# Kernel tuning notes

Measured on AMD Instinct MI355X. Metric: run time of the kernel, lower is better.

Reference implementation:

```python
import jax, jax.numpy as jnp
import numpy as np

B, T, N, CD, D = 8, 16, 256, 1280, 1024   # batch, frames, feats/frame, condition_dim, dim
H, DH, DEPTH, Q = 16, 64, 6, 16           # heads, dim_head, depth, latents per frame
FF = 4 * D


def setup_inputs() -> dict:
    key = jax.random.key(0)
    ks = iter(jax.random.split(key, 40))
    w = lambda shp: jax.random.normal(next(ks), shp, jnp.float32) * 0.02
    return dict(
        x_f=jax.random.normal(next(ks), (B, T, N, CD), jnp.float32),
        goal_w1=w((CD, 2 * D)), goal_b1=jnp.zeros((2 * D,), jnp.float32),
        goal_w2=w((2 * D, D)), goal_b2=jnp.zeros((D,), jnp.float32),
        latents=jax.random.normal(next(ks), (T, Q, D), jnp.float32),
        time_pos_emb=jax.random.normal(next(ks), (T, 1, D), jnp.float32),
        ln_media_g=jnp.ones((DEPTH, D), jnp.float32), ln_media_b=jnp.zeros((DEPTH, D), jnp.float32),
        ln_lat_g=jnp.ones((DEPTH, D), jnp.float32), ln_lat_b=jnp.zeros((DEPTH, D), jnp.float32),
        wq=w((DEPTH, D, H * DH)), wk=w((DEPTH, D, H * DH)), wv=w((DEPTH, D, H * DH)),
        wo=w((DEPTH, H * DH, D)),
        ffn_ln_g=jnp.ones((DEPTH, D), jnp.float32), ffn_ln_b=jnp.zeros((DEPTH, D), jnp.float32),
        ffn_w1=w((DEPTH, D, FF)), ffn_b1=jnp.zeros((DEPTH, FF), jnp.float32),
        ffn_w2=w((DEPTH, FF, D)), ffn_b2=jnp.zeros((DEPTH, D), jnp.float32),
        final_g=jnp.ones((D,), jnp.float32), final_b=jnp.zeros((D,), jnp.float32),
    )


def layer_norm(x, g, b, eps=1e-5):
    m = jnp.mean(x, axis=-1, keepdims=True)
    v = jnp.mean(jnp.square(x - m), axis=-1, keepdims=True)
    return (x - m) * jax.lax.rsqrt(v + eps) * g + b


def reference(x_f, goal_w1, goal_b1, goal_w2, goal_b2, latents, time_pos_emb,
              ln_media_g, ln_media_b, ln_lat_g, ln_lat_b, wq, wk, wv, wo,
              ffn_ln_g, ffn_ln_b, ffn_w1, ffn_b1, ffn_w2, ffn_b2, final_g, final_b):
    scale = DH ** -0.5
    # goal embedding: Linear -> GELU(exact) -> Linear, then add time positional embedding
    h = jax.nn.gelu(x_f @ goal_w1 + goal_b1, approximate=False) @ goal_w2 + goal_b2  # (B,T,N,D)
    h = h + time_pos_emb[None]                                                       # (T,1,D) broadcast
    feats = h.reshape(B * T, N, D)
    x = jnp.broadcast_to(latents[None], (B, T, Q, D)).reshape(B * T, Q, D)
    for i in range(DEPTH):
        f = layer_norm(feats, ln_media_g[i], ln_media_b[i])
        lat = layer_norm(x, ln_lat_g[i], ln_lat_b[i])
        q = (lat @ wq[i]).reshape(B * T, Q, H, DH).transpose(0, 2, 1, 3) * scale  # bhqd
        kv = jnp.concatenate([f, lat], axis=1)                                    # (BT, N+Q, D)
        k = (kv @ wk[i]).reshape(B * T, N + Q, H, DH).transpose(0, 2, 1, 3)       # bhfd
        v = (kv @ wv[i]).reshape(B * T, N + Q, H, DH).transpose(0, 2, 1, 3)
        sim = jnp.einsum('bhqd,bhfd->bhqf', q, k)
        alphas = jax.nn.softmax(sim, axis=-1)  # matches amax-subtract + softmax
        o = jnp.einsum('bhqf,bhfd->bhqd', alphas, v)
        o = o.transpose(0, 2, 1, 3).reshape(B * T, Q, H * DH)
        x = x + o @ wo[i]
        y = layer_norm(x, ffn_ln_g[i], ffn_ln_b[i])
        x = x + jax.nn.gelu(y @ ffn_w1[i] + ffn_b1[i], approximate=False) @ ffn_w2[i] + ffn_b2[i]
    x = x.reshape(B, T * Q, D)
    return layer_norm(x, final_g, final_b)
```

## Files before the change

kernel.cpp:

```cpp
#include <hip/hip_runtime.h>
#include <math.h>

#define DEV __device__ __forceinline__

typedef __attribute__((ext_vector_type(8))) short short8;
typedef __attribute__((ext_vector_type(4))) short short4v;
typedef __attribute__((ext_vector_type(4))) float f32x4;
typedef __attribute__((ext_vector_type(8))) __bf16 bf16x8;

DEV float bf2f(unsigned short u) {
    union { unsigned int i; float f; } c; c.i = ((unsigned int)u) << 16; return c.f;
}
DEV unsigned short f2bf(float f) {
    union { float f; unsigned int i; } c; c.f = f;
    unsigned int u = c.i;
    u += 0x7fffu + ((u >> 16) & 1u);
    return (unsigned short)(u >> 16);
}
DEV float gelu_exact(float x) { return 0.5f * x * (1.0f + erff(x * 0.70710678118654752f)); }

DEV f32x4 MF(bf16x8 a, bf16x8 b, f32x4 c) {
    return __builtin_amdgcn_mfma_f32_16x16x32_bf16(a, b, c, 0, 0, 0);
}

#define GLL16(g, l)                                                                   \
    __builtin_amdgcn_global_load_lds(                                                \
        (const __attribute__((address_space(1))) unsigned int*)(g),                  \
        (__attribute__((address_space(3))) unsigned int*)(l), 16, 0, 0)

__global__ __launch_bounds__(256)
void transpose_w(const float* __restrict__ in, unsigned short* __restrict__ out,
                 const float* __restrict__ rowscale, float uscale,
                 int K, int N, size_t inStride, size_t outStride, int scaleStride)
{
    __shared__ float tile[64][65];
    in  += (size_t)blockIdx.z * inStride;
    out += (size_t)blockIdx.z * outStride;
    const int k0 = blockIdx.y * 64, n0 = blockIdx.x * 64;
    const int tid = threadIdx.x;
    const int c = tid & 63;
#pragma unroll
    for (int i = 0; i < 16; ++i) {
        int rr = (i << 2) + (tid >> 6);
        float v = in[(size_t)(k0 + rr) * N + n0 + c];
        if (rowscale) v *= rowscale[(size_t)blockIdx.z * scaleStride + k0 + rr];
        tile[rr][c] = v * uscale;
    }
    __syncthreads();
#pragma unroll
    for (int i = 0; i < 16; ++i) {
        int rr = (i << 2) + (tid >> 6);
        out[(size_t)(n0 + rr) * K + k0 + c] = f2bf(tile[c][rr]);
    }
}

__global__ __launch_bounds__(256)
void fold_bias(const float* __restrict__ wk, const float* __restrict__ wv,
               const float* __restrict__ bmed, float* __restrict__ biaskv)
{
    const int d = blockIdx.x >> 3;
    const int rem = blockIdx.x & 7;
    const int part = rem >> 2;
    const int chunk = rem & 3;
    const float* w = (part ? wv : wk) + (size_t)d * 1024 * 1024 + chunk * 256 + threadIdx.x;
    const float* b = bmed + d * 1024;
    float acc = 0.f;
    for (int r = 0; r < 1024; ++r) acc += b[r] * w[(size_t)r * 1024];
    biaskv[d * 2048 + part * 1024 + chunk * 256 + threadIdx.x] = acc;
}

__global__ __launch_bounds__(256)
void convert_bf16(const float* __restrict__ in, unsigned short* __restrict__ out, size_t n4)
{
    size_t i = (size_t)blockIdx.x * 256 + threadIdx.x;
    if (i >= n4) return;
    float4 v = ((const float4*)in)[i];
    ushort4 u;
    u.x = f2bf(v.x); u.y = f2bf(v.y); u.z = f2bf(v.z); u.w = f2bf(v.w);
    ((ushort4*)out)[i] = u;
}

__global__ __launch_bounds__(256)
void init_x(const float* __restrict__ lat, float* __restrict__ x)
{
    const int row = blockIdx.x;
    ((float4*)x)[(size_t)row * 256 + threadIdx.x] =
        ((const float4*)lat)[(size_t)(row & 255) * 256 + threadIdx.x];
}

template<bool AFFINE, bool OUTBF>
__global__ __launch_bounds__(256)
void ln_k(const float* __restrict__ in, const float* __restrict__ g,
          const float* __restrict__ b, void* __restrict__ out)
{
    const int row = blockIdx.x;
    const int tid = threadIdx.x;
    float4 v = ((const float4*)(in + (size_t)row * 1024))[tid];
    float s  = v.x + v.y + v.z + v.w;
    float ss = v.x * v.x + v.y * v.y + v.z * v.z + v.w * v.w;
#pragma unroll
    for (int o = 32; o > 0; o >>= 1) { s += __shfl_down(s, o); ss += __shfl_down(ss, o); }
    __shared__ float red[8];
    if ((tid & 63) == 0) { red[tid >> 6] = s; red[4 + (tid >> 6)] = ss; }
    __syncthreads();
    const float sum  = red[0] + red[1] + red[2] + red[3];
    const float ssum = red[4] + red[5] + red[6] + red[7];
    const float mean = sum * (1.0f / 1024.0f);
    const float var  = ssum * (1.0f / 1024.0f) - mean * mean;
    const float rs   = rsqrtf(var + 1e-5f);
    float o0 = (v.x - mean) * rs, o1 = (v.y - mean) * rs;
    float o2 = (v.z - mean) * rs, o3 = (v.w - mean) * rs;
    if (AFFINE) {
        float4 gv = ((const float4*)g)[tid];
        float4 bv = ((const float4*)b)[tid];
        o0 = o0 * gv.x + bv.x; o1 = o1 * gv.y + bv.y;
        o2 = o2 * gv.z + bv.z; o3 = o3 * gv.w + bv.w;
    }
    if (OUTBF) {
        ushort4 u; u.x = f2bf(o0); u.y = f2bf(o1); u.z = f2bf(o2); u.w = f2bf(o3);
        ((ushort4*)out)[(size_t)row * 256 + tid] = u;
    } else {
        float4 ov; ov.x = o0; ov.y = o1; ov.z = o2; ov.w = o3;
        ((float4*)out)[(size_t)row * 256 + tid] = ov;
    }
}

enum { E_BF16 = 0, E_BIAS_BF16, E_BIAS_GELU_BF16, E_BIAS_TPOS_F32, E_ADD_F32, E_BIAS_ADD_F32 };

template<int EPI>
__global__ __launch_bounds__(256, 2)
void gemm_bt(const unsigned short* __restrict__ A, const unsigned short* __restrict__ Bt,
             void* __restrict__ Out,
             const float* __restrict__ bias, const float* __restrict__ addsrc,
             const float* __restrict__ tpos,
             int M, int N, int K)
{
    __shared__ unsigned short lds[2 * 128 * 64];
    const int tid  = threadIdx.x;
    const int wave = tid >> 6, lane = tid & 63;
    const int nbx  = N >> 7;

    const int nwg = gridDim.x;
    int bid = blockIdx.x;
    int wg = ((nwg & 7) == 0) ? ((bid & 7) * (nwg >> 3) + (bid >> 3)) : bid;
    const int by = wg / nbx, bx = wg % nbx;

    const int swz = ((lane & 7) ^ (lane >> 3)) * 8;
    const unsigned short* gA = A  + (size_t)(by * 128 + (lane >> 3)) * K + swz;
    const unsigned short* gB = Bt + (size_t)(bx * 128 + (lane >> 3)) * K + swz;

    const int wr = wave >> 1, wc = wave & 1;
    f32x4 acc[4][4] = {};

    unsigned short* ldsA = lds;
    unsigned short* ldsB = lds + 128 * 64;

    const int off0 = (((lane >> 4)    ) ^ (lane & 7)) * 8;
    const int off1 = (((lane >> 4) | 4) ^ (lane & 7)) * 8;
    const unsigned short* la = ldsA + (wr * 64 + (lane & 15)) * 64;
    const unsigned short* lb = ldsB + (wc * 64 + (lane & 15)) * 64;

    for (int kt = 0; kt < K; kt += 64) {
#pragma unroll
        for (int j = 0; j < 4; ++j) {
            const int chunk = (j << 2) + wave;
            GLL16(gA + (size_t)chunk * 8 * K + kt, ldsA + chunk * 512);
            GLL16(gB + (size_t)chunk * 8 * K + kt, ldsB + chunk * 512);
        }
        __syncthreads();
#pragma unroll
        for (int kk = 0; kk < 2; ++kk) {
            const int offk = kk ? off1 : off0;
            bf16x8 a[4], b[4];
#pragma unroll
            for (int m = 0; m < 4; ++m) a[m] = *(const bf16x8*)(la + m * 1024 + offk);
#pragma unroll
            for (int n = 0; n < 4; ++n) b[n] = *(const bf16x8*)(lb + n * 1024 + offk);
#pragma unroll
            for (int m = 0; m < 4; ++m)
#pragma unroll
                for (int n = 0; n < 4; ++n)
                    acc[m][n] = MF(a[m], b[n], acc[m][n]);
        }
        __syncthreads();
    }

    const int r0 = by * 128 + wr * 64 + (lane >> 4) * 4;
    const int c0 = bx * 128 + wc * 64 + (lane & 15);
#pragma unroll
    for (int m = 0; m < 4; ++m) {
#pragma unroll
        for (int n = 0; n < 4; ++n) {
            const int c = c0 + n * 16;
#pragma unroll
            for (int j = 0; j < 4; ++j) {
                const int r = r0 + m * 16 + j;
                float v = acc[m][n][j];
                if (EPI == E_BIAS_BF16 || EPI == E_BIAS_GELU_BF16 ||
                    EPI == E_BIAS_TPOS_F32 || EPI == E_BIAS_ADD_F32)
                    v += bias[c];
                if (EPI == E_BIAS_GELU_BF16) v = gelu_exact(v);
                if (EPI == E_BIAS_TPOS_F32)  v += tpos[(((unsigned)r >> 8) & 15) * 1024 + c];
                if (EPI == E_ADD_F32 || EPI == E_BIAS_ADD_F32) v += addsrc[(size_t)r * N + c];
                if (EPI == E_BIAS_TPOS_F32 || EPI == E_ADD_F32 || EPI == E_BIAS_ADD_F32)
                    ((float*)Out)[(size_t)r * N + c] = v;
                else
                    ((unsigned short*)Out)[(size_t)r * N + c] = f2bf(v);
            }
        }
    }
}

template<int EPI>
__global__ __launch_bounds__(256, 4)
void gemm64(const unsigned short* __restrict__ A, const unsigned short* __restrict__ Bt,
            void* __restrict__ Out,
            const float* __restrict__ bias, const float* __restrict__ addsrc,
            int M, int N, int K)
{
    __shared__ unsigned short lds[64 * 64 + 128 * 64];
    const int tid  = threadIdx.x;
    const int wave = tid >> 6, lane = tid & 63;
    const int nbx  = N >> 7;

    const int nwg = gridDim.x;
    int bid = blockIdx.x;
    int wg = ((nwg & 7) == 0) ? ((bid & 7) * (nwg >> 3) + (bid >> 3)) : bid;
    const int by = wg / nbx, bx = wg % nbx;

    const int swz = ((lane & 7) ^ (lane >> 3)) * 8;
    const unsigned short* gA = A  + (size_t)(by * 64  + (lane >> 3)) * K + swz;
    const unsigned short* gB = Bt + (size_t)(bx * 128 + (lane >> 3)) * K + swz;

    const int wr = wave >> 1, wc = wave & 1;
    f32x4 acc[2][4] = {};

    unsigned short* ldsA = lds;
    unsigned short* ldsB = lds + 64 * 64;

    const int off0 = (((lane >> 4)    ) ^ (lane & 7)) * 8;
    const int off1 = (((lane >> 4) | 4) ^ (lane & 7)) * 8;
    const unsigned short* la = ldsA + (wr * 32 + (lane & 15)) * 64;
    const unsigned short* lb = ldsB + (wc * 64 + (lane & 15)) * 64;

    for (int kt = 0; kt < K; kt += 64) {
        GLL16(gA + (size_t)(wave)     * 8 * K + kt, ldsA + (wave)      * 512);
        GLL16(gA + (size_t)(4 + wave) * 8 * K + kt, ldsA + (4 + wave)  * 512);
#pragma unroll
        for (int j = 0; j < 4; ++j) {
            const int chunk = (j << 2) + wave;
            GLL16(gB + (size_t)chunk * 8 * K + kt, ldsB + chunk * 512);
        }
        __syncthreads();
#pragma unroll
        for (int kk = 0; kk < 2; ++kk) {
            const int offk = kk ? off1 : off0;
            bf16x8 a[2], b[4];
#pragma unroll
            for (int m = 0; m < 2; ++m) a[m] = *(const bf16x8*)(la + m * 1024 + offk);
#pragma unroll
            for (int n = 0; n < 4; ++n) b[n] = *(const bf16x8*)(lb + n * 1024 + offk);
#pragma unroll
            for (int m = 0; m < 2; ++m)
#pragma unroll
                for (int n = 0; n < 4; ++n)
                    acc[m][n] = MF(a[m], b[n], acc[m][n]);
        }
        __syncthreads();
    }

    const int r0 = by * 64 + wr * 32 + (lane >> 4) * 4;
    const int c0 = bx * 128 + wc * 64 + (lane & 15);
#pragma unroll
    for (int m = 0; m < 2; ++m) {
#pragma unroll
        for (int n = 0; n < 4; ++n) {
            const int c = c0 + n * 16;
#pragma unroll
            for (int j = 0; j < 4; ++j) {
                const int r = r0 + m * 16 + j;
                float v = acc[m][n][j];
                if (EPI == E_BIAS_BF16 || EPI == E_BIAS_GELU_BF16 || EPI == E_BIAS_ADD_F32)
                    v += bias[c];
                if (EPI == E_BIAS_GELU_BF16) v = gelu_exact(v);
                if (EPI == E_ADD_F32 || EPI == E_BIAS_ADD_F32) v += addsrc[(size_t)r * N + c];
                if (EPI == E_ADD_F32 || EPI == E_BIAS_ADD_F32)
                    ((float*)Out)[(size_t)r * N + c] = v;
                else
                    ((unsigned short*)Out)[(size_t)r * N + c] = f2bf(v);
            }
        }
    }
}

template<int EPI>
__global__ __launch_bounds__(256, 4)
void gemm3232(const unsigned short* __restrict__ A, const unsigned short* __restrict__ Bt,
              void* __restrict__ Out,
              const float* __restrict__ bias, const float* __restrict__ addsrc,
              int M, int N, int K)
{
    __shared__ unsigned short lds[2 * 64 * 64];
    const int tid  = threadIdx.x;
    const int wave = tid >> 6, lane = tid & 63;
    const int nbx  = N >> 6;

    const int nwg = gridDim.x;
    int bid = blockIdx.x;
    int wg = ((nwg & 7) == 0) ? ((bid & 7) * (nwg >> 3) + (bid >> 3)) : bid;
    const int by = wg / nbx, bx = wg % nbx;

    const int swz = ((lane & 7) ^ (lane >> 3)) * 8;
    const unsigned short* gA = A  + (size_t)(by * 64 + (lane >> 3)) * K + swz;
    const unsigned short* gB = Bt + (size_t)(bx * 64 + (lane >> 3)) * K + swz;

    const int wr = wave >> 1, wc = wave & 1;
    f32x4 acc[2][2] = {};

    unsigned short* ldsA = lds;
    unsigned short* ldsB = lds + 64 * 64;

    const int off0 = (((lane >> 4)    ) ^ (lane & 7)) * 8;
    const int off1 = (((lane >> 4) | 4) ^ (lane & 7)) * 8;
    const unsigned short* la = ldsA + (wr * 32 + (lane & 15)) * 64;
    const unsigned short* lb = ldsB + (wc * 32 + (lane & 15)) * 64;

    for (int kt = 0; kt < K; kt += 64) {
        GLL16(gA + (size_t)(wave)     * 8 * K + kt, ldsA + (wave)      * 512);
        GLL16(gA + (size_t)(4 + wave) * 8 * K + kt, ldsA + (4 + wave)  * 512);
        GLL16(gB + (size_t)(wave)     * 8 * K + kt, ldsB + (wave)      * 512);
        GLL16(gB + (size_t)(4 + wave) * 8 * K + kt, ldsB + (4 + wave)  * 512);
        __syncthreads();
#pragma unroll
        for (int kk = 0; kk < 2; ++kk) {
            const int offk = kk ? off1 : off0;
            bf16x8 a[2], b[2];
#pragma unroll
            for (int m = 0; m < 2; ++m) a[m] = *(const bf16x8*)(la + m * 1024 + offk);
#pragma unroll
            for (int n = 0; n < 2; ++n) b[n] = *(const bf16x8*)(lb + n * 1024 + offk);
#pragma unroll
            for (int m = 0; m < 2; ++m)
#pragma unroll
                for (int n = 0; n < 2; ++n)
                    acc[m][n] = MF(a[m], b[n], acc[m][n]);
        }
        __syncthreads();
    }

    const int r0 = by * 64 + wr * 32 + (lane >> 4) * 4;
    const int c0 = bx * 64 + wc * 32 + (lane & 15);
#pragma unroll
    for (int m = 0; m < 2; ++m) {
#pragma unroll
        for (int n = 0; n < 2; ++n) {
            const int c = c0 + n * 16;
#pragma unroll
            for (int j = 0; j < 4; ++j) {
                const int r = r0 + m * 16 + j;
                float v = acc[m][n][j];
                if (EPI == E_BIAS_BF16 || EPI == E_BIAS_GELU_BF16 || EPI == E_BIAS_ADD_F32)
                    v += bias[c];
                if (EPI == E_BIAS_GELU_BF16) v = gelu_exact(v);
                if (EPI == E_ADD_F32 || EPI == E_BIAS_ADD_F32) v += addsrc[(size_t)r * N + c];
                if (EPI == E_ADD_F32 || EPI == E_BIAS_ADD_F32)
                    ((float*)Out)[(size_t)r * N + c] = v;
                else
                    ((unsigned short*)Out)[(size_t)r * N + c] = f2bf(v);
            }
        }
    }
}

__global__ __launch_bounds__(256)
void attn_k(const unsigned short* __restrict__ qkvl, const unsigned short* __restrict__ kvm,
            unsigned short* __restrict__ o)
{
    __shared__ unsigned short kv[272 * 72];
    __shared__ float sim[16 * 273];
    __shared__ float qs[16 * 68];
    __shared__ float red[64];

    const int bt = blockIdx.x >> 4, h = blockIdx.x & 15;
    const int tid = threadIdx.x;
    const int lane = tid & 63, wave = tid >> 6;
    const int r = tid & 15, grp = tid >> 4;

    {
        const int qi = tid >> 4, d0 = (tid & 15) * 4;
        const unsigned short* src = qkvl + (size_t)(bt * 16 + qi) * 3072 + h * 64 + d0;
        qs[qi * 68 + d0 + 0] = bf2f(src[0]);
        qs[qi * 68 + d0 + 1] = bf2f(src[1]);
        qs[qi * 68 + d0 + 2] = bf2f(src[2]);
        qs[qi * 68 + d0 + 3] = bf2f(src[3]);
    }
#pragma unroll
    for (int i = 0; i < 9; ++i) {
        int idx = i * 256 + tid;
        if (idx < 2176) {
            int f = idx >> 3, cp = idx & 7;
            const unsigned short* src = (f < 256)
                ? kvm  + (size_t)(bt * 256 + f) * 2048 + h * 64 + cp * 8
                : qkvl + (size_t)(bt * 16 + (f - 256)) * 3072 + 1024 + h * 64 + cp * 8;
            *(short8*)&kv[f * 72 + cp * 8] = *(const short8*)src;
        }
    }
    __syncthreads();

    float p[17];
#pragma unroll
    for (int i = 0; i < 17; ++i) p[i] = 0.f;
#pragma unroll
    for (int d = 0; d < 64; d += 8) {
        float q8[8];
#pragma unroll
        for (int j = 0; j < 8; ++j) q8[j] = qs[r * 68 + d + j];
#pragma unroll
        for (int i = 0; i < 17; ++i) {
            short8 k8 = *(const short8*)&kv[(grp + i * 16) * 72 + d];
#pragma unroll
            for (int j = 0; j < 8; ++j) p[i] += q8[j] * bf2f((unsigned short)k8[j]);
        }
    }
    float mx = -3.0e38f;
#pragma unroll
    for (int i = 0; i < 17; ++i) mx = fmaxf(mx, p[i]);
    mx = fmaxf(mx, __shfl_xor(mx, 16));
    mx = fmaxf(mx, __shfl_xor(mx, 32));
    if (lane < 16) red[wave * 16 + lane] = mx;
    __syncthreads();
    const float rowmax = fmaxf(fmaxf(red[r], red[16 + r]), fmaxf(red[32 + r], red[48 + r]));

    float sm = 0.f;
#pragma unroll
    for (int i = 0; i < 17; ++i) { p[i] = __expf(p[i] - rowmax); sm += p[i]; }
    sm += __shfl_xor(sm, 16);
    sm += __shfl_xor(sm, 32);
#pragma unroll
    for (int i = 0; i < 17; ++i) sim[r * 273 + grp + i * 16] = p[i];
    __syncthreads();
    if (lane < 16) red[wave * 16 + lane] = sm;
#pragma unroll
    for (int i = 0; i < 9; ++i) {
        int idx = i * 256 + tid;
        if (idx < 2176) {
            int f = idx >> 3, cp = idx & 7;
            const unsigned short* src = (f < 256)
                ? kvm  + (size_t)(bt * 256 + f) * 2048 + 1024 + h * 64 + cp * 8
                : qkvl + (size_t)(bt * 16 + (f - 256)) * 3072 + 2048 + h * 64 + cp * 8;
            *(short8*)&kv[f * 72 + cp * 8] = *(const short8*)src;
        }
    }
    __syncthreads();
    const float inv = 1.0f / (red[r] + red[16 + r] + red[32 + r] + red[48 + r]);

    float o0 = 0.f, o1 = 0.f, o2 = 0.f, o3 = 0.f;
    for (int f = 0; f < 272; ++f) {
        float pv = sim[r * 273 + f];
        short4v v4 = *(const short4v*)&kv[f * 72 + grp * 4];
        o0 += pv * bf2f((unsigned short)v4[0]);
        o1 += pv * bf2f((unsigned short)v4[1]);
        o2 += pv * bf2f((unsigned short)v4[2]);
        o3 += pv * bf2f((unsigned short)v4[3]);
    }
    unsigned short* dst = o + (size_t)(bt * 16 + r) * 1024 + h * 64 + grp * 4;
    dst[0] = f2bf(o0 * inv);
    dst[1] = f2bf(o1 * inv);
    dst[2] = f2bf(o2 * inv);
    dst[3] = f2bf(o3 * inv);
}

extern "C" void kernel_launch(void* const* d_in, const int* in_sizes, int n_in,
                              void* d_out, int out_size, void* d_ws, size_t ws_size,
                              hipStream_t stream)
{
    const float* x_f      = (const float*)d_in[0];
    const float* goal_w1  = (const float*)d_in[1];
    const float* goal_b1  = (const float*)d_in[2];
    const float* goal_w2  = (const float*)d_in[3];
    const float* goal_b2  = (const float*)d_in[4];
    const float* latents  = (const float*)d_in[5];
    const float* tpos     = (const float*)d_in[6];
    const float* lnm_g    = (const float*)d_in[7];
    const float* lnm_b    = (const float*)d_in[8];
    const float* lnl_g    = (const float*)d_in[9];
    const float* lnl_b    = (const float*)d_in[10];
    const float* wq       = (const float*)d_in[11];
    const float* wk       = (const float*)d_in[12];
    const float* wv       = (const float*)d_in[13];
    const float* wo       = (const float*)d_in[14];
    const float* ffn_g    = (const float*)d_in[15];
    const float* ffn_b    = (const float*)d_in[16];
    const float* ffw1     = (const float*)d_in[17];
    const float* ffb1     = (const float*)d_in[18];
    const float* ffw2     = (const float*)d_in[19];
    const float* ffb2     = (const float*)d_in[20];
    const float* fin_g    = (const float*)d_in[21];
    const float* fin_b    = (const float*)d_in[22];

    char* ws = (char*)d_ws;
    size_t off = 0;
    auto alloc = [&](size_t bytes) -> char* {
        char* p = ws + off;
        off += (bytes + 255) & ~(size_t)255;
        return p;
    };
    typedef unsigned short u16;
    u16*   wg1t   = (u16*)  alloc(2048ull * 1280 * 2);
    u16*   wg2t   = (u16*)  alloc(1024ull * 2048 * 2);
    u16*   wqkvl  = (u16*)  alloc(6ull * 3072 * 1024 * 2);
    u16*   wkvm   = (u16*)  alloc(6ull * 2048 * 1024 * 2);
    u16*   wot    = (u16*)  alloc(6ull * 1024 * 1024 * 2);
    u16*   wf1t   = (u16*)  alloc(6ull * 4096 * 1024 * 2);
    u16*   wf2t   = (u16*)  alloc(6ull * 1024 * 4096 * 2);
    float* biaskv = (float*)alloc(6ull * 2048 * 4);
    float* xres   = (float*)alloc(2048ull * 1024 * 4);
    u16*   latn   = (u16*)  alloc(2048ull * 1024 * 2);
    u16*   qkvl   = (u16*)  alloc(2048ull * 3072 * 2);
    u16*   obuf   = (u16*)  alloc(2048ull * 1024 * 2);
    u16*   ffny   = (u16*)  alloc(2048ull * 1024 * 2);
    u16*   ffnmid = (u16*)  alloc(2048ull * 4096 * 2);
    u16*   bufA   = (u16*)  alloc(32768ull * 2048 * 2);
    float* bufB   = (float*)alloc(32768ull * 1024 * 4);
    u16*   bufC   = (u16*)  alloc(41943040ull * 2);
    if (off > ws_size) return;

    convert_bf16<<<40960, 256, 0, stream>>>(x_f, bufC, 41943040ull / 4);
    transpose_w<<<dim3(32, 20, 1), 256, 0, stream>>>(goal_w1, wg1t, nullptr, 1.f, 1280, 2048, 0, 0, 0);
    transpose_w<<<dim3(16, 32, 1), 256, 0, stream>>>(goal_w2, wg2t, nullptr, 1.f, 2048, 1024, 0, 0, 0);
    transpose_w<<<dim3(16, 16, 6), 256, 0, stream>>>(wq, wqkvl,                nullptr, 0.125f, 1024, 1024, 1024ull*1024, 3072ull*1024, 0);
    transpose_w<<<dim3(16, 16, 6), 256, 0, stream>>>(wk, wqkvl + 1024ull*1024, nullptr, 1.f,    1024, 1024, 1024ull*1024, 3072ull*1024, 0);
    transpose_w<<<dim3(16, 16, 6), 256, 0, stream>>>(wv, wqkvl + 2048ull*1024, nullptr, 1.f,    1024, 1024, 1024ull*1024, 3072ull*1024, 0);
    transpose_w<<<dim3(16, 16, 6), 256, 0, stream>>>(wk, wkvm,                 lnm_g,   1.f,    1024, 1024, 1024ull*1024, 2048ull*1024, 1024);
    transpose_w<<<dim3(16, 16, 6), 256, 0, stream>>>(wv, wkvm + 1024ull*1024,  lnm_g,   1.f,    1024, 1024, 1024ull*1024, 2048ull*1024, 1024);
    transpose_w<<<dim3(16, 16, 6), 256, 0, stream>>>(wo, wot,                  nullptr, 1.f,    1024, 1024, 1024ull*1024, 1024ull*1024, 0);
    transpose_w<<<dim3(64, 16, 6), 256, 0, stream>>>(ffw1, wf1t,               nullptr, 1.f,    1024, 4096, 4096ull*1024, 4096ull*1024, 0);
    transpose_w<<<dim3(16, 64, 6), 256, 0, stream>>>(ffw2, wf2t,               nullptr, 1.f,    4096, 1024, 4096ull*1024, 4096ull*1024, 0);
    fold_bias<<<48, 256, 0, stream>>>(wk, wv, lnm_b, biaskv);
    init_x<<<2048, 256, 0, stream>>>(latents, xres);

    gemm_bt<E_BIAS_GELU_BF16><<<256 * 16, 256, 0, stream>>>(bufC, wg1t, bufA, goal_b1, nullptr, nullptr, 32768, 2048, 1280);
    gemm_bt<E_BIAS_TPOS_F32><<<256 * 8, 256, 0, stream>>>(bufA, wg2t, bufB, goal_b2, nullptr, tpos, 32768, 1024, 2048);
    ln_k<false, true><<<32768, 256, 0, stream>>>(bufB, nullptr, nullptr, bufC);

    for (int i = 0; i < 6; ++i) {
        const u16* wqkvl_i = wqkvl + (size_t)i * 3072 * 1024;
        const u16* wkvm_i  = wkvm  + (size_t)i * 2048 * 1024;
        const u16* wot_i   = wot   + (size_t)i * 1024 * 1024;
        const u16* wf1_i   = wf1t  + (size_t)i * 4096 * 1024;
        const u16* wf2_i   = wf2t  + (size_t)i * 1024 * 4096;

        ln_k<true, true><<<2048, 256, 0, stream>>>(xres, lnl_g + i * 1024, lnl_b + i * 1024, latn);
        gemm64<E_BF16><<<32 * 24, 256, 0, stream>>>(latn, wqkvl_i, qkvl, nullptr, nullptr, 2048, 3072, 1024);
        gemm_bt<E_BIAS_BF16><<<256 * 16, 256, 0, stream>>>(bufC, wkvm_i, bufA, biaskv + i * 2048, nullptr, nullptr, 32768, 2048, 1024);
        attn_k<<<2048, 256, 0, stream>>>(qkvl, bufA, obuf);
        gemm3232<E_ADD_F32><<<32 * 16, 256, 0, stream>>>(obuf, wot_i, xres, nullptr, xres, 2048, 1024, 1024);
        ln_k<true, true><<<2048, 256, 0, stream>>>(xres, ffn_g + i * 1024, ffn_b + i * 1024, ffny);
        gemm64<E_BIAS_GELU_BF16><<<32 * 32, 256, 0, stream>>>(ffny, wf1_i, ffnmid, ffb1 + i * 4096, nullptr, 2048, 4096, 1024);
        gemm3232<E_BIAS_ADD_F32><<<32 * 16, 256, 0, stream>>>(ffnmid, wf2_i, xres, ffb2 + i * 1024, xres, 2048, 1024, 4096);
    }

    ln_k<true, false><<<2048, 256, 0, stream>>>(xres, fin_g, fin_b, d_out);
}
```

Measured before the change: 2.735 ms.

## Double-buffer LDS in large GEMM to overlap global loads with MFMA

Replaces the single-buffered 128x128 GEMM with a two-phase version that prefetches the next K tile into a second LDS buffer while computing on the current one, using one barrier per iteration instead of two. K becomes a template parameter so address arithmetic and loop trip counts are compile-time constants. MFMA sections run at raised wave priority, and the bias load is hoisted out of the inner epilogue loop. LDS use doubles to 64 KB per block, which may limit residency at two blocks per CU.

```diff
diff --git a/kernel.cpp b/kernel.cpp
--- a/kernel.cpp
+++ b/kernel.cpp
@@ -27,6 +27,11 @@
     __builtin_amdgcn_global_load_lds(                                                \
         (const __attribute__((address_space(1))) unsigned int*)(g),                  \
         (__attribute__((address_space(3))) unsigned int*)(l), 16, 0, 0)
+
+#define BAR()     __builtin_amdgcn_s_barrier()
+#define VMCNT(n)  asm volatile("s_waitcnt vmcnt(" #n ")" ::: "memory")
+#define LGKM(n)   do { asm volatile("s_waitcnt lgkmcnt(" #n ")" ::: "memory");        \
+                       __builtin_amdgcn_sched_barrier(0); } while (0)
 
 __global__ __launch_bounds__(256)
 void transpose_w(const float* __restrict__ in, unsigned short* __restrict__ out,
@@ -127,15 +132,14 @@
 
 enum { E_BF16 = 0, E_BIAS_BF16, E_BIAS_GELU_BF16, E_BIAS_TPOS_F32, E_ADD_F32, E_BIAS_ADD_F32 };
 
-template<int EPI>
+template<int EPI, int K>
 __global__ __launch_bounds__(256, 2)
-void gemm_bt(const unsigned short* __restrict__ A, const unsigned short* __restrict__ Bt,
+void gemm2ph(const unsigned short* __restrict__ A, const unsigned short* __restrict__ Bt,
              void* __restrict__ Out,
-             const float* __restrict__ bias, const float* __restrict__ addsrc,
-             const float* __restrict__ tpos,
-             int M, int N, int K)
-{
-    __shared__ unsigned short lds[2 * 128 * 64];
+             const float* __restrict__ bias, const float* __restrict__ tpos,
+             int M, int N)
+{
+    __shared__ unsigned short lds[2 * 16384];
     const int tid  = threadIdx.x;
     const int wave = tid >> 6, lane = tid & 63;
     const int nbx  = N >> 7;
@@ -152,37 +156,62 @@
     const int wr = wave >> 1, wc = wave & 1;
     f32x4 acc[4][4] = {};
 
-    unsigned short* ldsA = lds;
-    unsigned short* ldsB = lds + 128 * 64;
+    auto stage = [&](int buf, int t) {
+        unsigned short* dA = lds + buf * 16384;
+        unsigned short* dB = dA + 8192;
+        const size_t kt = (size_t)t * 64;
+#pragma unroll
+        for (int j = 0; j < 4; ++j) {
+            const int chunk = (j << 2) + wave;
+            GLL16(gA + (size_t)chunk * 8 * K + kt, dA + chunk * 512);
+            GLL16(gB + (size_t)chunk * 8 * K + kt, dB + chunk * 512);
+        }
+    };
 
     const int off0 = (((lane >> 4)    ) ^ (lane & 7)) * 8;
     const int off1 = (((lane >> 4) | 4) ^ (lane & 7)) * 8;
-    const unsigned short* la = ldsA + (wr * 64 + (lane & 15)) * 64;
-    const unsigned short* lb = ldsB + (wc * 64 + (lane & 15)) * 64;
-
-    for (int kt = 0; kt < K; kt += 64) {
-#pragma unroll
-        for (int j = 0; j < 4; ++j) {
-            const int chunk = (j << 2) + wave;
-            GLL16(gA + (size_t)chunk * 8 * K + kt, ldsA + chunk * 512);
-            GLL16(gB + (size_t)chunk * 8 * K + kt, ldsB + chunk * 512);
-        }
-        __syncthreads();
-#pragma unroll
-        for (int kk = 0; kk < 2; ++kk) {
-            const int offk = kk ? off1 : off0;
-            bf16x8 a[4], b[4];
-#pragma unroll
-            for (int m = 0; m < 4; ++m) a[m] = *(const bf16x8*)(la + m * 1024 + offk);
-#pragma unroll
-            for (int n = 0; n < 4; ++n) b[n] = *(const bf16x8*)(lb + n * 1024 + offk);
+    const int aro  = (wr * 64 + (lane & 15)) * 64;
+    const int bro  = 8192 + (wc * 64 + (lane & 15)) * 64;
+
+    const int nt = K >> 6;
+
+    stage(0, 0);
+    VMCNT(0);
+    BAR();
+
+    for (int t = 0; t < nt; ++t) {
+        const int cur = t & 1;
+        const bool s1 = (t + 1 < nt);
+        if (s1) stage(cur ^ 1, t + 1);
+
+        const unsigned short* la = lds + cur * 16384 + aro;
+        const unsigned short* lb = lds + cur * 16384 + bro;
+        bf16x8 a[2][4], b[2][4];
+#pragma unroll
+        for (int m = 0; m < 4; ++m) {
+            a[0][m] = *(const bf16x8*)(la + m * 1024 + off0);
+            a[1][m] = *(const bf16x8*)(la + m * 1024 + off1);
+        }
+#pragma unroll
+        for (int n = 0; n < 4; ++n) {
+            b[0][n] = *(const bf16x8*)(lb + n * 1024 + off0);
+            b[1][n] = *(const bf16x8*)(lb + n * 1024 + off1);
+        }
+        LGKM(0);
+        __builtin_amdgcn_s_setprio(1);
+#pragma unroll
+        for (int kk = 0; kk < 2; ++kk)
 #pragma unroll
             for (int m = 0; m < 4; ++m)
 #pragma unroll
                 for (int n = 0; n < 4; ++n)
-                    acc[m][n] = MF(a[m], b[n], acc[m][n]);
-        }
-        __syncthreads();
+                    acc[m][n] = MF(a[kk][m], b[kk][n], acc[m][n]);
+        __builtin_amdgcn_s_setprio(0);
+
+        if (s1) {
+            VMCNT(0);
+            BAR();
+        }
     }
 
     const int r0 = by * 128 + wr * 64 + (lane >> 4) * 4;
@@ -192,20 +221,20 @@
 #pragma unroll
         for (int n = 0; n < 4; ++n) {
             const int c = c0 + n * 16;
+            float bv = 0.f;
+            if (EPI == E_BIAS_BF16 || EPI == E_BIAS_GELU_BF16 || EPI == E_BIAS_TPOS_F32)
+                bv = bias[c];
 #pragma unroll
             for (int j = 0; j < 4; ++j) {
                 const int r = r0 + m * 16 + j;
-                float v = acc[m][n][j];
-                if (EPI == E_BIAS_BF16 || EPI == E_BIAS_GELU_BF16 ||
-                    EPI == E_BIAS_TPOS_F32 || EPI == E_BIAS_ADD_F32)
-                    v += bias[c];
+                float v = acc[m][n][j] + bv;
                 if (EPI == E_BIAS_GELU_BF16) v = gelu_exact(v);
-                if (EPI == E_BIAS_TPOS_F32)  v += tpos[(((unsigned)r >> 8) & 15) * 1024 + c];
-                if (EPI == E_ADD_F32 || EPI == E_BIAS_ADD_F32) v += addsrc[(size_t)r * N + c];
-                if (EPI == E_BIAS_TPOS_F32 || EPI == E_ADD_F32 || EPI == E_BIAS_ADD_F32)
+                if (EPI == E_BIAS_TPOS_F32) {
+                    v += tpos[(((unsigned)r >> 8) & 15) * 1024 + c];
                     ((float*)Out)[(size_t)r * N + c] = v;
-                else
+                } else {
                     ((unsigned short*)Out)[(size_t)r * N + c] = f2bf(v);
+                }
             }
         }
     }
@@ -539,8 +568,8 @@
     fold_bias<<<48, 256, 0, stream>>>(wk, wv, lnm_b, biaskv);
     init_x<<<2048, 256, 0, stream>>>(latents, xres);
 
-    gemm_bt<E_BIAS_GELU_BF16><<<256 * 16, 256, 0, stream>>>(bufC, wg1t, bufA, goal_b1, nullptr, nullptr, 32768, 2048, 1280);
-    gemm_bt<E_BIAS_TPOS_F32><<<256 * 8, 256, 0, stream>>>(bufA, wg2t, bufB, goal_b2, nullptr, tpos, 32768, 1024, 2048);
+    gemm2ph<E_BIAS_GELU_BF16, 1280><<<256 * 16, 256, 0, stream>>>(bufC, wg1t, bufA, goal_b1, nullptr, 32768, 2048);
+    gemm2ph<E_BIAS_TPOS_F32, 2048><<<256 * 8, 256, 0, stream>>>(bufA, wg2t, bufB, goal_b2, tpos, 32768, 1024);
     ln_k<false, true><<<32768, 256, 0, stream>>>(bufB, nullptr, nullptr, bufC);
 
     for (int i = 0; i < 6; ++i) {
@@ -552,7 +581,7 @@
 
         ln_k<true, true><<<2048, 256, 0, stream>>>(xres, lnl_g + i * 1024, lnl_b + i * 1024, latn);
         gemm64<E_BF16><<<32 * 24, 256, 0, stream>>>(latn, wqkvl_i, qkvl, nullptr, nullptr, 2048, 3072, 1024);
-        gemm_bt<E_BIAS_BF16><<<256 * 16, 256, 0, stream>>>(bufC, wkvm_i, bufA, biaskv + i * 2048, nullptr, nullptr, 32768, 2048, 1024);
+        gemm2ph<E_BIAS_BF16, 1024><<<256 * 16, 256, 0, stream>>>(bufC, wkvm_i, bufA, biaskv + i * 2048, nullptr, 32768, 2048);
         attn_k<<<2048, 256, 0, stream>>>(qkvl, bufA, obuf);
         gemm3232<E_ADD_F32><<<32 * 16, 256, 0, stream>>>(obuf, wot_i, xres, nullptr, xres, 2048, 1024, 1024);
         ln_k<true, true><<<2048, 256, 0, stream>>>(xres, ffn_g + i * 1024, ffn_b + i * 1024, ffny);
```

Result: slower. 2.905 ms (+6.2%).
